# Kernel tuning notes

Measured on AMD Instinct MI355X. Metric: run time of the kernel, lower is better.

Reference implementation:

```python
import jax, jax.numpy as jnp
import numpy as np

NUM_HEADS = 12
NUM_FRAMES = 8
WINDOW = (14, 14)


def _gen_relative_position_index(ws):
    h, w = ws
    num_rel = (2 * h - 1) * (2 * w - 1) + 3
    area = h * w
    coords = np.stack(np.meshgrid(np.arange(h), np.arange(w), indexing='ij'))  # (2,h,w)
    cf = coords.reshape(2, -1)
    rel = cf[:, :, None] - cf[:, None, :]  # (2,A,A)
    rel = rel.transpose(1, 2, 0).astype(np.int64)
    rel[:, :, 0] += h - 1
    rel[:, :, 1] += w - 1
    rel[:, :, 0] *= 2 * w - 1
    idx = np.zeros((area + 1, area + 1), dtype=np.int32)
    idx[1:, 1:] = rel.sum(-1)
    idx[0, :] = num_rel - 3
    idx[:, 0] = num_rel - 2
    idx[0, 0] = num_rel - 1
    return idx


def _gen_relative_temporal_index(nf):
    c = np.arange(nf)
    return (c[:, None] - c[None, :] + nf - 1).astype(np.int32)


def setup_inputs() -> dict:
    key = jax.random.key(0)
    ks = jax.random.split(key, 8)
    B, N, C = 2, NUM_FRAMES * WINDOW[0] * WINDOW[1], 768  # N = 1568
    num_rel = (2 * WINDOW[0] - 1) * (2 * WINDOW[1] - 1) + 3  # 732
    return {
        'x': jax.random.normal(ks[0], (B, N, C), jnp.float32),
        'qkv_w': jax.random.normal(ks[1], (3 * C, C), jnp.float32) * 0.02,
        'q_bias': jax.random.normal(ks[2], (C,), jnp.float32) * 0.02,
        'v_bias': jax.random.normal(ks[3], (C,), jnp.float32) * 0.02,
        'rel_pos_table': jax.random.normal(ks[4], (num_rel, NUM_HEADS), jnp.float32) * 0.02,
        'rel_temp_table': jax.random.normal(ks[5], (2 * NUM_FRAMES - 1, NUM_HEADS), jnp.float32) * 0.02,
        'proj_w': jax.random.normal(ks[6], (C, C), jnp.float32) * 0.02,
        'proj_b': jax.random.normal(ks[7], (C,), jnp.float32) * 0.02,
        'rel_pos_index': jnp.asarray(_gen_relative_position_index(WINDOW)),
        'rel_temp_index': jnp.asarray(_gen_relative_temporal_index(NUM_FRAMES)),
    }


def reference(x, qkv_w, q_bias, v_bias, rel_pos_table, rel_temp_table, proj_w, proj_b,
              rel_pos_index, rel_temp_index):
    B, N, C = x.shape
    H = NUM_HEADS
    D = C // H
    scale = D ** -0.5
    nf = NUM_FRAMES

    # qkv projection with concat(q_bias, zeros(k), v_bias)
    qkv_bias = jnp.concatenate([q_bias, jnp.zeros_like(q_bias), v_bias])
    qkv = x @ qkv_w.T + qkv_bias  # [B,N,3C]
    qkv = qkv.reshape(B, N, 3, H, D).transpose(2, 0, 3, 1, 4)  # [3,B,H,N,D]
    q, k, v = qkv[0], qkv[1], qkv[2]

    attn = jnp.einsum('bhqd,bhkd->bhqk', q * scale, k)  # [B,H,N,N]

    # gathered 2D relative position bias, tiled over frames, sliced to N
    rel = rel_pos_table[rel_pos_index]  # [197,197,H]
    rel = jnp.transpose(rel, (2, 0, 1))[None]  # [1,H,197,197]
    rel = jnp.tile(rel, (1, 1, nf, nf))[:, :, :N, :N]
    attn = attn + rel

    # temporal bias, repeat_interleave by tokens-per-frame
    tpf = N // nf  # 196
    temp = rel_temp_table[rel_temp_index]  # [nf,nf,H]
    temp = jnp.transpose(temp, (2, 0, 1))[None]  # [1,H,nf,nf]
    temp = jnp.repeat(jnp.repeat(temp, tpf, axis=2), tpf, axis=3)  # [1,H,N,N]
    attn = attn + temp

    attn = jax.nn.softmax(attn, axis=-1)
    attn = jnp.nan_to_num(attn, nan=0.0)

    out = jnp.einsum('bhqk,bhkd->bhqd', attn, v)  # [B,H,N,D]
    out = out.transpose(0, 2, 1, 3).reshape(B, N, C)
    return out @ proj_w.T + proj_b
```

## Files before the change

kernel.cpp:

```cpp
#include <hip/hip_runtime.h>
#include <hip/hip_bf16.h>

#define NHEADS 12
#define NFRAMES 8
#define NTOK 1568
#define CDIM 768
#define DHEAD 64
#define BATCH 2
#define MROWS (BATCH * NTOK)
#define MPAD 3200
#define K3 (3 * CDIM)
#define AREA1 197
#define TPF 196
#define LOG2E 1.4426950408889634f

typedef __bf16 bf16x8 __attribute__((ext_vector_type(8)));
typedef float f32x4 __attribute__((ext_vector_type(4)));
typedef float f32x16 __attribute__((ext_vector_type(16)));
typedef unsigned short u16x8 __attribute__((ext_vector_type(8)));

#if __has_builtin(__builtin_amdgcn_exp2f)
#define EXP2(x) __builtin_amdgcn_exp2f(x)
#else
#define EXP2(x) exp2f(x)
#endif

__device__ __forceinline__ unsigned short f2bf(float f) {
  return __builtin_bit_cast(unsigned short, (__bf16)f);
}
__device__ __forceinline__ float bf2f(unsigned short u) {
  unsigned int x = ((unsigned int)u) << 16;
  return __builtin_bit_cast(float, x);
}
__device__ __forceinline__ bf16x8 ld8(const unsigned short* p) {
  return __builtin_bit_cast(bf16x8, *(const u16x8*)p);
}
__device__ __forceinline__ f32x4 mfma16(bf16x8 a, bf16x8 b, f32x4 c) {
  return __builtin_amdgcn_mfma_f32_16x16x32_bf16(a, b, c, 0, 0, 0);
}
__device__ __forceinline__ f32x16 mfma32(bf16x8 a, bf16x8 b, f32x16 c) {
  return __builtin_amdgcn_mfma_f32_32x32x16_bf16(a, b, c, 0, 0, 0);
}
__device__ __forceinline__ unsigned int pack2(float lo, float hi) {
  return ((unsigned int)f2bf(hi) << 16) | (unsigned int)f2bf(lo);
}
__device__ __forceinline__ void swap32(unsigned int a, unsigned int b,
                                       unsigned int& x, unsigned int& y) {
#if __has_builtin(__builtin_amdgcn_permlane32_swap)
  auto r = __builtin_amdgcn_permlane32_swap(a, b, false, false);
  x = r[0]; y = r[1];
#else
  const bool hi = (threadIdx.x & 63) >= 32;
  unsigned int ea = (unsigned int)__shfl_xor((int)a, 32);
  unsigned int eb = (unsigned int)__shfl_xor((int)b, 32);
  x = hi ? eb : a;
  y = hi ? b : ea;
#endif
}
#define GL_LDS(src, dst)                                                    \
  __builtin_amdgcn_global_load_lds(                                         \
      (const __attribute__((address_space(1))) void*)(src),                 \
      (__attribute__((address_space(3))) void*)(dst), 16, 0, 0)

__device__ __forceinline__ int xcd_swz(int lin, int nwg) {
  const int q = nwg >> 3, r = nwg & 7;
  const int xcd = lin & 7, idx = lin >> 3;
  return (xcd < r ? xcd * (q + 1) : r * (q + 1) + (xcd - r) * q) + idx;
}

__global__ void conv_kernel(const float* __restrict__ x,
                            const float* __restrict__ qkv_w,
                            const float* __restrict__ proj_w,
                            unsigned short* __restrict__ xb,
                            unsigned short* __restrict__ qkvwb,
                            unsigned short* __restrict__ projwb,
                            unsigned short* __restrict__ aout) {
  const int XCH = MPAD * CDIM / 4;
  const int WCH = K3 * CDIM / 4;
  const int PCH = CDIM * CDIM / 4;
  const int ACH = (MPAD - MROWS) * CDIM / 4;
  const int total = XCH + WCH + PCH + ACH;
  for (int c = blockIdx.x * blockDim.x + threadIdx.x; c < total;
       c += gridDim.x * blockDim.x) {
    if (c < XCH) {
      int m = (c * 4) / CDIM;
      float4 v = make_float4(0.f, 0.f, 0.f, 0.f);
      if (m < MROWS) v = ((const float4*)x)[c];
      ushort4 o;
      o.x = f2bf(v.x); o.y = f2bf(v.y); o.z = f2bf(v.z); o.w = f2bf(v.w);
      ((ushort4*)xb)[c] = o;
    } else if (c < XCH + WCH) {
      int c2 = c - XCH;
      float4 v = ((const float4*)qkv_w)[c2];
      ushort4 o;
      o.x = f2bf(v.x); o.y = f2bf(v.y); o.z = f2bf(v.z); o.w = f2bf(v.w);
      ((ushort4*)qkvwb)[c2] = o;
    } else if (c < XCH + WCH + PCH) {
      int c2 = c - XCH - WCH;
      float4 v = ((const float4*)proj_w)[c2];
      ushort4 o;
      o.x = f2bf(v.x); o.y = f2bf(v.y); o.z = f2bf(v.z); o.w = f2bf(v.w);
      ((ushort4*)projwb)[c2] = o;
    } else {
      int c2 = c - XCH - WCH - PCH;
      ushort4 z; z.x = 0; z.y = 0; z.z = 0; z.w = 0;
      ((ushort4*)(aout + (size_t)MROWS * CDIM))[c2] = z;
    }
  }
}

__global__ void biasP_kernel(const float* __restrict__ rpt,
                             const int* __restrict__ rpi,
                             const float* __restrict__ rtt,
                             const int* __restrict__ rti,
                             unsigned short* __restrict__ biasP,
                             float* __restrict__ bias2) {
  if (blockIdx.x == NHEADS * AREA1) {
    int t = threadIdx.x;
    for (; t < NHEADS * 64; t += 256) {
      int h = t >> 6, ff = t & 63;
      bias2[t] = rtt[rti[ff] * NHEADS + h] * LOG2E;
    }
    return;
  }
  __shared__ float row[AREA1];
  const int h = blockIdx.x / AREA1;
  const int i = blockIdx.x - h * AREA1;
  for (int j = threadIdx.x; j < AREA1; j += 256)
    row[j] = rpt[rpi[i * AREA1 + j] * NHEADS + h] * LOG2E;
  __syncthreads();
  unsigned short* dst = biasP + (size_t)blockIdx.x * 49 * 32;
  for (int e = threadIdx.x; e < 49 * 32; e += 256) {
    const int t = e >> 5, r = e & 31;
    const int hi = r >> 4, rr = r & 15;
    int km = 32 * t + (rr & 3) + 8 * (rr >> 2) + 4 * hi;
    km %= AREA1;
    dst[e] = f2bf(row[km]);
  }
}

template <int MODE, int BM, int BN, int TPB, int WAVES_M, int NB_N>
__global__ __launch_bounds__(TPB) void gemm_kernel(
    const unsigned short* __restrict__ A,
    const unsigned short* __restrict__ Bw,
    const float* __restrict__ bias0,
    const float* __restrict__ biasv,
    unsigned short* __restrict__ qbuf,
    unsigned short* __restrict__ kbuf,
    unsigned short* __restrict__ vtbuf,
    float* __restrict__ Cout) {
  constexpr int WAVES = TPB / 64;
  constexpr int WAVES_N = WAVES / WAVES_M;
  constexpr int WM = BM / WAVES_M;
  constexpr int WN = BN / WAVES_N;
  __shared__ unsigned short As[2][BM * 32];
  __shared__ unsigned short Bs[2][BN * 32];
  const int lane = threadIdx.x & 63;
  const int wv = threadIdx.x >> 6;
  const int tid = threadIdx.x;
  const int wg = xcd_swz(blockIdx.x, gridDim.x);
  const int m0 = (wg / NB_N) * BM;
  const int n0 = (wg % NB_N) * BN;

  auto stage = [&](int buf, int kt) {
    const int k0 = kt * 32;
#pragma unroll
    for (int ai = 0; ai < BM * 32 / (TPB * 8); ++ai) {
      const int c = ai * TPB + tid;
      const int r = c >> 2, seg = c & 3;
      GL_LDS(A + (size_t)(m0 + r) * CDIM + k0 + seg * 8, &As[buf][c * 8]);
    }
#pragma unroll
    for (int bi = 0; bi < BN * 32 / (TPB * 8); ++bi) {
      const int c = bi * TPB + tid;
      const int r = c >> 2, seg = c & 3;
      GL_LDS(Bw + (size_t)(n0 + r) * CDIM + k0 + seg * 8, &Bs[buf][c * 8]);
    }
  };

  f32x4 acc[WM / 16][WN / 16] = {};
  const int rbase = (wv & (WAVES_M - 1)) * WM;
  const int cbase = (wv / WAVES_M) * WN;

  stage(0, 0);
  __syncthreads();
  int cur = 0;
  for (int kt = 0; kt < CDIM / 32; ++kt) {
    if (kt + 1 < CDIM / 32) stage(cur ^ 1, kt + 1);
    bf16x8 af[WM / 16], bg[WN / 16];
#pragma unroll
    for (int i = 0; i < WM / 16; ++i)
      af[i] = ld8(&As[cur][(rbase + i * 16 + (lane & 15)) * 32 + (lane >> 4) * 8]);
#pragma unroll
    for (int j = 0; j < WN / 16; ++j)
      bg[j] = ld8(&Bs[cur][(cbase + j * 16 + (lane & 15)) * 32 + (lane >> 4) * 8]);
#pragma unroll
    for (int i = 0; i < WM / 16; ++i)
#pragma unroll
      for (int j = 0; j < WN / 16; ++j)
        acc[i][j] = mfma16(af[i], bg[j], acc[i][j]);
    __syncthreads();
    cur ^= 1;
  }

#pragma unroll
  for (int i = 0; i < WM / 16; ++i) {
#pragma unroll
    for (int j = 0; j < WN / 16; ++j) {
#pragma unroll
      for (int r = 0; r < 4; ++r) {
        int grow = m0 + rbase + i * 16 + (lane >> 4) * 4 + r;
        int gcol = n0 + cbase + j * 16 + (lane & 15);
        if (grow >= MROWS) continue;
        float v = acc[i][j][r];
        if (MODE == 0) {
          int which = gcol / CDIM;
          int cc = gcol - which * CDIM;
          int hh = cc >> 6, dd = cc & 63;
          int b = grow / NTOK, n = grow - b * NTOK;
          size_t hd = ((size_t)(b * NHEADS + hh) * NTOK + n) * 64 + dd;
          if (which == 0)
            qbuf[hd] = f2bf((v + bias0[cc]) * (0.125f * LOG2E));
          else if (which == 1)
            kbuf[hd] = f2bf(v);
          else
            vtbuf[((size_t)(b * NHEADS + hh) * 64 + dd) * NTOK + n] =
                f2bf(v + biasv[cc]);
        } else {
          Cout[(size_t)grow * CDIM + gcol] = v + bias0[gcol];
        }
      }
    }
  }
}

__global__ __launch_bounds__(256) void attn_kernel(
    const unsigned short* __restrict__ qbuf,
    const unsigned short* __restrict__ kbuf,
    const unsigned short* __restrict__ vtbuf,
    const unsigned short* __restrict__ biasP,
    const float* __restrict__ bias2,
    unsigned short* __restrict__ aout) {
  __shared__ __align__(16) char smem[36864];
  unsigned short* stg = (unsigned short*)smem;
  float* mb = (float*)smem;

  const int lane = threadIdx.x & 63;
  const int wv = threadIdx.x >> 6;
  const int wu = (blockIdx.x & 7) * 147 + (blockIdx.x >> 3);
  const int bh = wu / 49;
  const int qt = wu - bh * 49;
  const int q0 = qt * 32;
  const int h = bh % NHEADS;
  const int b = bh / NHEADS;
  const int qlane = lane & 31;
  const int hi = lane >> 5;
  const int hi4 = hi * 4;
  const int qn = q0 + qlane;
  const int qfr = qn / TPF < 7 ? qn / TPF : 7;
  const int qmod = qn % AREA1;

  const unsigned short* qp = qbuf + (size_t)bh * NTOK * DHEAD;
  const unsigned short* kp = kbuf + (size_t)bh * NTOK * DHEAD;
  const unsigned short* vp = vtbuf + (size_t)bh * DHEAD * NTOK;
  const unsigned short* bP = biasP + ((size_t)(h * AREA1 + qmod) * 49) * 32 + hi * 16;
  const float* b2q = bias2 + h * 64 + qfr * 8;

  unsigned short* KsW = stg + wv * 4096;
  unsigned short* VsW = KsW + 2048;

  const unsigned short* ksb =
      kp + (size_t)(lane >> 3) * DHEAD + (((lane & 7) ^ (lane >> 3)) << 3);
  const unsigned short* vsb =
      vp + (size_t)(lane >> 2) * NTOK + (((lane & 3) ^ ((lane >> 3) & 3)) << 3);

  auto stage = [&](int gt) {
    const int kv0 = gt * 32;
#pragma unroll
    for (int j = 0; j < 4; ++j) {
      GL_LDS(ksb + (size_t)(kv0 + j * 8) * DHEAD, KsW + j * 512);
      GL_LDS(vsb + kv0 + (size_t)(j * 16) * NTOK, VsW + j * 512);
    }
  };

  bf16x8 aq[4];
#pragma unroll
  for (int c = 0; c < 4; ++c)
    aq[c] = ld8(qp + (size_t)qn * DHEAD + c * 16 + hi * 8);

  f32x16 o0 = {}, o1 = {};
  float lrun = 0.f;

  stage(wv);
  u16x8 ubA, ubB;
  {
    const u16x8* bp = (const u16x8*)(bP + (size_t)wv * 32);
    ubA = bp[0]; ubB = bp[1];
  }
  int kfl = 0;
  float b2lo = b2q[0], b2hi = b2q[1];
  const int skey = qlane & 7;
  const int vswz = (qlane >> 1) & 3;

  for (int gt = wv; gt < 49; gt += 4) {
    asm volatile("s_waitcnt vmcnt(0)" ::: "memory");
    __builtin_amdgcn_sched_barrier(0);
    bf16x8 kf[4];
#pragma unroll
    for (int c = 0; c < 4; ++c)
      kf[c] = ld8(&KsW[qlane * 64 + ((((c << 1) + hi) ^ skey) << 3)]);
    bf16x8 vf0 = ld8(&VsW[qlane * 32 + ((hi ^ vswz) << 3)]);
    bf16x8 vf1 = ld8(&VsW[qlane * 32 + (((2 + hi) ^ vswz) << 3)]);
    bf16x8 vf2 = ld8(&VsW[(32 + qlane) * 32 + ((hi ^ vswz) << 3)]);
    bf16x8 vf3 = ld8(&VsW[(32 + qlane) * 32 + (((2 + hi) ^ vswz) << 3)]);
    asm volatile("s_waitcnt lgkmcnt(0)" ::: "memory");
    __builtin_amdgcn_sched_barrier(0);
    const bool more = (gt + 4 < 49);
    if (more) stage(gt + 4);

    f32x16 s;
#pragma unroll
    for (int r = 0; r < 16; ++r)
      s[r] = ((r < 8) ? bf2f(ubA[r]) : bf2f(ubB[r - 8])) + b2lo;
    __builtin_amdgcn_s_setprio(1);
#pragma unroll
    for (int c = 0; c < 4; ++c) s = mfma32(kf[c], aq[c], s);
    __builtin_amdgcn_s_setprio(0);

    const int ccr = (kfl + 1) * TPF - gt * 32;
    int kfln = kfl;
    float nb2lo = b2lo, nb2hi = b2hi;
    if (more) {
      const u16x8* bp = (const u16x8*)(bP + (size_t)(gt + 4) * 32);
      ubA = bp[0]; ubB = bp[1];
      kfln = ((gt + 4) * 8) / 49;
      nb2lo = b2q[kfln];
      nb2hi = b2q[kfln < 7 ? kfln + 1 : 7];
    }

    if (ccr < 32) {
      const float dlt = b2hi - b2lo;
#pragma unroll
      for (int r = 0; r < 16; ++r)
        s[r] += ((r & 3) + 8 * (r >> 2) + hi4 >= ccr) ? dlt : 0.f;
    }

#pragma unroll
    for (int r = 0; r < 16; ++r) s[r] = EXP2(s[r]);
    float ps;
    {
      float a = (s[0] + s[1]) + (s[2] + s[3]);
      float bb = (s[4] + s[5]) + (s[6] + s[7]);
      float cc = (s[8] + s[9]) + (s[10] + s[11]);
      float dd = (s[12] + s[13]) + (s[14] + s[15]);
      ps = (a + bb) + (cc + dd);
    }
    {
      unsigned int px, py;
      swap32(__builtin_bit_cast(unsigned int, ps),
             __builtin_bit_cast(unsigned int, ps), px, py);
      ps = __builtin_bit_cast(float, px) + __builtin_bit_cast(float, py);
    }
    lrun += ps;

    unsigned int dw[8];
#pragma unroll
    for (int c = 0; c < 8; ++c) dw[c] = pack2(s[2 * c], s[2 * c + 1]);
    unsigned int f0[4], f1[4];
    swap32(dw[0], dw[2], f0[0], f0[2]);
    swap32(dw[1], dw[3], f0[1], f0[3]);
    swap32(dw[4], dw[6], f1[0], f1[2]);
    swap32(dw[5], dw[7], f1[1], f1[3]);
    const bf16x8 F0 = __builtin_bit_cast(bf16x8, *(ulonglong2*)f0);
    const bf16x8 F1 = __builtin_bit_cast(bf16x8, *(ulonglong2*)f1);

    __builtin_amdgcn_s_setprio(1);
    o0 = mfma32(vf0, F0, o0);
    o0 = mfma32(vf1, F1, o0);
    o1 = mfma32(vf2, F0, o1);
    o1 = mfma32(vf3, F1, o1);
    __builtin_amdgcn_s_setprio(0);

    kfl = kfln;
    b2lo = nb2lo;
    b2hi = nb2hi;
  }

  __syncthreads();
  float* mrow = mb + (size_t)(wv * 64 + lane) * 34;
#pragma unroll
  for (int r = 0; r < 16; ++r) {
    mrow[r] = o0[r];
    mrow[16 + r] = o1[r];
  }
  mrow[32] = lrun;
  __syncthreads();
  if (wv < 2) {
    const int off = wv * 16;
    float acc[16];
#pragma unroll
    for (int r = 0; r < 16; ++r) acc[r] = 0.f;
    float L = 0.f;
#pragma unroll
    for (int w2 = 0; w2 < 4; ++w2) {
      const float* rr = mb + (size_t)(w2 * 64 + lane) * 34;
      L += rr[32];
#pragma unroll
      for (int r = 0; r < 16; ++r) acc[r] += rr[off + r];
    }
    const float rinv = 1.0f / L;
    unsigned short* op = aout + (size_t)(b * NTOK + qn) * CDIM + h * 64 + wv * 32;
#pragma unroll
    for (int c = 0; c < 8; ++c) {
      const int d0 = 8 * (c >> 1) + 4 * hi + 2 * (c & 1);
      *(unsigned int*)(op + d0) = pack2(acc[2 * c] * rinv, acc[2 * c + 1] * rinv);
    }
  }
}

extern "C" void kernel_launch(void* const* d_in, const int* in_sizes, int n_in,
                              void* d_out, int out_size, void* d_ws, size_t ws_size,
                              hipStream_t stream) {
  (void)in_sizes; (void)n_in; (void)out_size; (void)ws_size;
  const float* x        = (const float*)d_in[0];
  const float* qkv_w    = (const float*)d_in[1];
  const float* q_bias   = (const float*)d_in[2];
  const float* v_bias   = (const float*)d_in[3];
  const float* rp_table = (const float*)d_in[4];
  const float* rt_table = (const float*)d_in[5];
  const float* proj_w   = (const float*)d_in[6];
  const float* proj_b   = (const float*)d_in[7];
  const int* rp_index   = (const int*)d_in[8];
  const int* rt_index   = (const int*)d_in[9];

  char* ws = (char*)d_ws;
  unsigned short* xb     = (unsigned short*)(ws);
  unsigned short* qkvwb  = (unsigned short*)(ws + 4915200);
  unsigned short* projwb = (unsigned short*)(ws + 8454144);
  unsigned short* qbuf   = (unsigned short*)(ws + 9633792);
  unsigned short* kbuf   = (unsigned short*)(ws + 14450688);
  unsigned short* vtbuf  = (unsigned short*)(ws + 19267584);
  unsigned short* aout   = (unsigned short*)(ws + 24084480);
  unsigned short* biasP  = (unsigned short*)(ws);
  float* bias2           = (float*)(ws + 30247424);

  conv_kernel<<<2048, 256, 0, stream>>>(x, qkv_w, proj_w, xb, qkvwb, projwb, aout);
  gemm_kernel<0, 128, 128, 512, 4, K3 / 128>
      <<<dim3((K3 / 128) * (MPAD / 128)), 512, 0, stream>>>(
          xb, qkvwb, q_bias, v_bias, qbuf, kbuf, vtbuf, nullptr);
  biasP_kernel<<<NHEADS * AREA1 + 1, 256, 0, stream>>>(
      rp_table, rp_index, rt_table, rt_index, biasP, bias2);
  attn_kernel<<<dim3(1176), 256, 0, stream>>>(
      qbuf, kbuf, vtbuf, biasP, bias2, aout);
  gemm_kernel<1, 64, 64, 256, 2, CDIM / 64>
      <<<dim3((CDIM / 64) * (MPAD / 64)), 256, 0, stream>>>(
          aout, projwb, proj_b, nullptr, nullptr, nullptr, nullptr, (float*)d_out);
}
```

Before: 121.0 us.

## Fuse fp32-to-bf16 conversion into GEMM tile staging and drop conversion kernel

Removes the separate conversion pass that turned x, qkv_w and proj_w into bf16 copies and zeroed the attention-output padding. The GEMMs now read fp32 operands into registers, convert them, and write bf16 tiles into LDS after the MFMA work of each step, so the next tile's loads overlap with compute. Padding rows are handled by clamping the A row index instead of zero-filled buffers. In exchange, the GEMMs read twice the bytes per operand and lose the direct global-to-LDS loads for the converted operands, and register pressure rises.

```diff
diff --git a/kernel.cpp b/kernel.cpp
--- a/kernel.cpp
+++ b/kernel.cpp
@@ -66,47 +66,6 @@
   const int q = nwg >> 3, r = nwg & 7;
   const int xcd = lin & 7, idx = lin >> 3;
   return (xcd < r ? xcd * (q + 1) : r * (q + 1) + (xcd - r) * q) + idx;
-}
-
-__global__ void conv_kernel(const float* __restrict__ x,
-                            const float* __restrict__ qkv_w,
-                            const float* __restrict__ proj_w,
-                            unsigned short* __restrict__ xb,
-                            unsigned short* __restrict__ qkvwb,
-                            unsigned short* __restrict__ projwb,
-                            unsigned short* __restrict__ aout) {
-  const int XCH = MPAD * CDIM / 4;
-  const int WCH = K3 * CDIM / 4;
-  const int PCH = CDIM * CDIM / 4;
-  const int ACH = (MPAD - MROWS) * CDIM / 4;
-  const int total = XCH + WCH + PCH + ACH;
-  for (int c = blockIdx.x * blockDim.x + threadIdx.x; c < total;
-       c += gridDim.x * blockDim.x) {
-    if (c < XCH) {
-      int m = (c * 4) / CDIM;
-      float4 v = make_float4(0.f, 0.f, 0.f, 0.f);
-      if (m < MROWS) v = ((const float4*)x)[c];
-      ushort4 o;
-      o.x = f2bf(v.x); o.y = f2bf(v.y); o.z = f2bf(v.z); o.w = f2bf(v.w);
-      ((ushort4*)xb)[c] = o;
-    } else if (c < XCH + WCH) {
-      int c2 = c - XCH;
-      float4 v = ((const float4*)qkv_w)[c2];
-      ushort4 o;
-      o.x = f2bf(v.x); o.y = f2bf(v.y); o.z = f2bf(v.z); o.w = f2bf(v.w);
-      ((ushort4*)qkvwb)[c2] = o;
-    } else if (c < XCH + WCH + PCH) {
-      int c2 = c - XCH - WCH;
-      float4 v = ((const float4*)proj_w)[c2];
-      ushort4 o;
-      o.x = f2bf(v.x); o.y = f2bf(v.y); o.z = f2bf(v.z); o.w = f2bf(v.w);
-      ((ushort4*)projwb)[c2] = o;
-    } else {
-      int c2 = c - XCH - WCH - PCH;
-      ushort4 z; z.x = 0; z.y = 0; z.z = 0; z.w = 0;
-      ((ushort4*)(aout + (size_t)MROWS * CDIM))[c2] = z;
-    }
-  }
 }
 
 __global__ void biasP_kernel(const float* __restrict__ rpt,
@@ -141,8 +100,9 @@
 
 template <int MODE, int BM, int BN, int TPB, int WAVES_M, int NB_N>
 __global__ __launch_bounds__(TPB) void gemm_kernel(
-    const unsigned short* __restrict__ A,
-    const unsigned short* __restrict__ Bw,
+    const float* __restrict__ Afp,
+    const unsigned short* __restrict__ Abf,
+    const float* __restrict__ Bfp,
     const float* __restrict__ bias0,
     const float* __restrict__ biasv,
     unsigned short* __restrict__ qbuf,
@@ -153,6 +113,7 @@
   constexpr int WAVES_N = WAVES / WAVES_M;
   constexpr int WM = BM / WAVES_M;
   constexpr int WN = BN / WAVES_N;
+  static_assert(BM * 4 == TPB && BN * 4 == TPB, "one chunk per thread");
   __shared__ unsigned short As[2][BM * 32];
   __shared__ unsigned short Bs[2][BN * 32];
   const int lane = threadIdx.x & 63;
@@ -162,31 +123,46 @@
   const int m0 = (wg / NB_N) * BM;
   const int n0 = (wg % NB_N) * BN;
 
-  auto stage = [&](int buf, int kt) {
-    const int k0 = kt * 32;
-#pragma unroll
-    for (int ai = 0; ai < BM * 32 / (TPB * 8); ++ai) {
-      const int c = ai * TPB + tid;
-      const int r = c >> 2, seg = c & 3;
-      GL_LDS(A + (size_t)(m0 + r) * CDIM + k0 + seg * 8, &As[buf][c * 8]);
-    }
-#pragma unroll
-    for (int bi = 0; bi < BN * 32 / (TPB * 8); ++bi) {
-      const int c = bi * TPB + tid;
-      const int r = c >> 2, seg = c & 3;
-      GL_LDS(Bw + (size_t)(n0 + r) * CDIM + k0 + seg * 8, &Bs[buf][c * 8]);
-    }
+  const int srow = tid >> 2, sseg = tid & 3;
+  int arow = m0 + srow; if (arow >= MROWS) arow = MROWS - 1;
+  const int brow = n0 + srow;
+
+  f32x4 ra0, ra1, rb0, rb1;
+  auto issueLoads = [&](int kt, int buf) {
+    const int k0 = kt * 32 + sseg * 8;
+    if (MODE == 0) {
+      const f32x4* ap = (const f32x4*)(Afp + (size_t)arow * CDIM + k0);
+      ra0 = ap[0]; ra1 = ap[1];
+    } else {
+      GL_LDS(Abf + (size_t)arow * CDIM + k0, &As[buf][tid * 8]);
+    }
+    const f32x4* bp = (const f32x4*)(Bfp + (size_t)brow * CDIM + k0);
+    rb0 = bp[0]; rb1 = bp[1];
+  };
+  auto writeStage = [&](int buf) {
+    u16x8 w;
+    if (MODE == 0) {
+      w[0] = f2bf(ra0[0]); w[1] = f2bf(ra0[1]); w[2] = f2bf(ra0[2]);
+      w[3] = f2bf(ra0[3]); w[4] = f2bf(ra1[0]); w[5] = f2bf(ra1[1]);
+      w[6] = f2bf(ra1[2]); w[7] = f2bf(ra1[3]);
+      *(u16x8*)&As[buf][tid * 8] = w;
+    }
+    w[0] = f2bf(rb0[0]); w[1] = f2bf(rb0[1]); w[2] = f2bf(rb0[2]);
+    w[3] = f2bf(rb0[3]); w[4] = f2bf(rb1[0]); w[5] = f2bf(rb1[1]);
+    w[6] = f2bf(rb1[2]); w[7] = f2bf(rb1[3]);
+    *(u16x8*)&Bs[buf][tid * 8] = w;
   };
 
   f32x4 acc[WM / 16][WN / 16] = {};
   const int rbase = (wv & (WAVES_M - 1)) * WM;
   const int cbase = (wv / WAVES_M) * WN;
 
-  stage(0, 0);
+  issueLoads(0, 0);
+  writeStage(0);
   __syncthreads();
   int cur = 0;
   for (int kt = 0; kt < CDIM / 32; ++kt) {
-    if (kt + 1 < CDIM / 32) stage(cur ^ 1, kt + 1);
+    if (kt + 1 < CDIM / 32) issueLoads(kt + 1, cur ^ 1);
     bf16x8 af[WM / 16], bg[WN / 16];
 #pragma unroll
     for (int i = 0; i < WM / 16; ++i)
@@ -199,6 +175,7 @@
 #pragma unroll
       for (int j = 0; j < WN / 16; ++j)
         acc[i][j] = mfma16(af[i], bg[j], acc[i][j]);
+    if (kt + 1 < CDIM / 32) writeStage(cur ^ 1);
     __syncthreads();
     cur ^= 1;
   }
@@ -434,9 +411,6 @@
   const int* rt_index   = (const int*)d_in[9];
 
   char* ws = (char*)d_ws;
-  unsigned short* xb     = (unsigned short*)(ws);
-  unsigned short* qkvwb  = (unsigned short*)(ws + 4915200);
-  unsigned short* projwb = (unsigned short*)(ws + 8454144);
   unsigned short* qbuf   = (unsigned short*)(ws + 9633792);
   unsigned short* kbuf   = (unsigned short*)(ws + 14450688);
   unsigned short* vtbuf  = (unsigned short*)(ws + 19267584);
@@ -444,15 +418,15 @@
   unsigned short* biasP  = (unsigned short*)(ws);
   float* bias2           = (float*)(ws + 30247424);
 
-  conv_kernel<<<2048, 256, 0, stream>>>(x, qkv_w, proj_w, xb, qkvwb, projwb, aout);
   gemm_kernel<0, 128, 128, 512, 4, K3 / 128>
       <<<dim3((K3 / 128) * (MPAD / 128)), 512, 0, stream>>>(
-          xb, qkvwb, q_bias, v_bias, qbuf, kbuf, vtbuf, nullptr);
+          x, nullptr, qkv_w, q_bias, v_bias, qbuf, kbuf, vtbuf, nullptr);
   biasP_kernel<<<NHEADS * AREA1 + 1, 256, 0, stream>>>(
       rp_table, rp_index, rt_table, rt_index, biasP, bias2);
   attn_kernel<<<dim3(1176), 256, 0, stream>>>(
       qbuf, kbuf, vtbuf, biasP, bias2, aout);
   gemm_kernel<1, 64, 64, 256, 2, CDIM / 64>
       <<<dim3((CDIM / 64) * (MPAD / 64)), 256, 0, stream>>>(
-          aout, projwb, proj_b, nullptr, nullptr, nullptr, nullptr, (float*)d_out);
-}
+          nullptr, aout, proj_w, proj_b, nullptr, nullptr, nullptr, nullptr,
+          (float*)d_out);
+}
```

Measured after the change: 123.5 us. 1.02x slower.
